# Kernel tuning notes

Measured on AMD Instinct MI355X. Metric: run time of the kernel, lower is better.

Reference implementation:

```python
import jax, jax.numpy as jnp
import numpy as np

N = 10000   # num nodes
E = 320000  # num edges (avg degree 32)
F = 128     # feat_size
H = 128     # hidden_size


def setup_inputs() -> dict:
    key = jax.random.key(0)
    ks = jax.random.split(key, 16)

    def p(k, shape, scale=0.05):
        return jax.random.normal(k, shape, jnp.float32) * scale

    inp = {
        "x": p(ks[0], (N, F), 1.0),
        "edge_index": jax.random.randint(ks[1], (2, E), 0, N),
    }
    # 6 SAGEConv layers: encoder (F->H, H->H), attr decoder (H->H, H->F),
    # struct decoder (H->H, H->N). Each has W_l (neighbor), b_l, W_r (root).
    dims = [(F, H), (H, H), (H, H), (H, F), (H, H), (H, N)]
    names = ["e1", "e2", "a1", "a2", "s1", "s2"]
    i = 2
    for name, (din, dout) in zip(names, dims):
        inp[f"Wl_{name}"] = p(ks[i], (din, dout))
        inp[f"bl_{name}"] = jnp.zeros((dout,), jnp.float32)
        inp[f"Wr_{name}"] = p(ks[i + 1], (din, dout))
        i += 2
    return inp


def sage(x, src, dst, Wl, bl, Wr, n):
    # PyG SAGEConv (aggr='mean'): mean of source-node features at each target,
    # then out = agg @ W_l + b + x @ W_r (root weight).
    msg = jax.ops.segment_sum(x[src], dst, num_segments=n)          # [n, din]
    deg = jax.ops.segment_sum(jnp.ones((src.shape[0],), x.dtype), dst, num_segments=n)
    agg = msg / jnp.maximum(deg, 1.0)[:, None]
    return agg @ Wl + bl + x @ Wr


def reference(x, edge_index,
              Wl_e1, bl_e1, Wr_e1, Wl_e2, bl_e2, Wr_e2,
              Wl_a1, bl_a1, Wr_a1, Wl_a2, bl_a2, Wr_a2,
              Wl_s1, bl_s1, Wr_s1, Wl_s2, bl_s2, Wr_s2):
    src, dst = edge_index[0], edge_index[1]
    n = x.shape[0]
    # Encoder (dropout is identity in eval mode)
    h = jax.nn.relu(sage(x, src, dst, Wl_e1, bl_e1, Wr_e1, n))
    h = jax.nn.relu(sage(h, src, dst, Wl_e2, bl_e2, Wr_e2, n))
    # Attribute decoder -> x_hat [N, F]
    xh = jax.nn.relu(sage(h, src, dst, Wl_a1, bl_a1, Wr_a1, n))
    xh = jax.nn.relu(sage(xh, src, dst, Wl_a2, bl_a2, Wr_a2, n))
    # Structure decoder -> [N, N], transposed as in the original
    s = jax.nn.relu(sage(h, src, dst, Wl_s1, bl_s1, Wr_s1, n))
    s = jax.nn.relu(sage(s, src, dst, Wl_s2, bl_s2, Wr_s2, n)).T
    return (s, xh)
```

## Files before the change

### kernel.cpp

```cpp
#include <hip/hip_runtime.h>
#include <hip/hip_bf16.h>

typedef unsigned short ushort_t;
typedef unsigned int uint_t;
typedef __attribute__((ext_vector_type(8))) short short8;
typedef __attribute__((ext_vector_type(4))) float float4v;

__device__ __forceinline__ float bf2f(ushort_t u) {
    union { uint_t i; float f; } c; c.i = ((uint_t)u) << 16; return c.f;
}
__device__ __forceinline__ ushort_t f2bf(float f) {
    union { float f; uint_t i; } c; c.f = f;
    uint_t x = c.i;
    uint_t r = x + 0x7fffu + ((x >> 16) & 1u);
    return (ushort_t)(r >> 16);
}

__device__ __forceinline__ void gl_lds16(const void* g, void* l) {
    __builtin_amdgcn_global_load_lds(
        (const __attribute__((address_space(1))) void*)g,
        (__attribute__((address_space(3))) void*)l, 16, 0, 0);
}

__device__ __forceinline__ void stv(float* p, float v) { *p = v; }
__device__ __forceinline__ void stv(ushort_t* p, float v) { *p = f2bf(v); }

__global__ __launch_bounds__(1024) void scan_kernel(
    const int* __restrict__ cnt, int* __restrict__ rowptr,
    int* __restrict__ cursor, float* __restrict__ deginv, int n) {
    __shared__ int sums[1024];
    const int t = threadIdx.x;
    const int per = (n + 1023) >> 10;
    const int b0 = t * per;
    int s = 0;
    for (int u = 0; u < per; u++) {
        int i = b0 + u;
        if (i < n) s += cnt[i];
    }
    sums[t] = s;
    __syncthreads();
    int x = s;
    for (int off = 1; off < 1024; off <<= 1) {
        int y = (t >= off) ? sums[t - off] : 0;
        __syncthreads();
        x += y;
        sums[t] = x;
        __syncthreads();
    }
    int run = x - s;
    for (int u = 0; u < per; u++) {
        int i = b0 + u;
        if (i < n) {
            int v = cnt[i];
            rowptr[i] = run;
            cursor[i] = run;
            deginv[i] = 1.0f / (float)(v > 0 ? v : 1);
            run += v;
        }
    }
    if (t == 1023) rowptr[n] = x;
}

__global__ void scatter_kernel(const int* __restrict__ srcv, const int* __restrict__ dstv,
                               int* __restrict__ cursor, int* __restrict__ srcs_sorted, int E) {
    int e = blockIdx.x * 256 + threadIdx.x;
    if (e < E) {
        int p = atomicAdd(&cursor[dstv[e]], 1);
        srcs_sorted[p] = srcv[e];
    }
}

struct W5 { const float* W0[5]; const float* W1[5]; };

__global__ __launch_bounds__(256) void setup_kernel(
    W5 wp, ushort_t* __restrict__ WT,
    const float* __restrict__ Ws2_0, const float* __restrict__ Ws2_1,
    ushort_t* __restrict__ WTs2, int Nout, int nbx,
    const int* __restrict__ dstv, int* __restrict__ cnt, int E) {
    __shared__ ushort_t tile[64][72];
    const int b = blockIdx.x;
    const int tid = threadIdx.x;
    if (b < 40) {
        const int bx = b & 1, by = (b >> 1) & 3, layer = b >> 3;
        const int i0 = bx * 64, k0 = by * 64;
        const float* W = (k0 < 128) ? (wp.W0[layer] + (size_t)k0 * 128)
                                    : (wp.W1[layer] + (size_t)(k0 - 128) * 128);
        ushort_t* WTb = WT + (size_t)layer * 128 * 256;
        const int li = tid & 63;
        const int kq = tid >> 6;
        const int gi = i0 + li;
        for (int k = kq; k < 64; k += 4)
            tile[li][k] = f2bf(W[(size_t)k * 128 + gi]);
        __syncthreads();
        for (int s = tid; s < 512; s += 256) {
            int r = s >> 3, ch = s & 7;
            *(short8*)(WTb + (size_t)(i0 + r) * 256 + k0 + ch * 8) = *(const short8*)&tile[r][ch * 8];
        }
    } else if (b < 40 + nbx * 4) {
        const int vt = b - 40;
        const int bx = vt % nbx, by = vt / nbx;
        const int i0 = bx * 64, k0 = by * 64;
        const float* W = (k0 < 128) ? (Ws2_0 + (size_t)k0 * Nout)
                                    : (Ws2_1 + (size_t)(k0 - 128) * Nout);
        const int li = tid & 63;
        const int kq = tid >> 6;
        const int gi = i0 + li;
        const bool ok = gi < Nout;
        for (int k = kq; k < 64; k += 4) {
            float v = ok ? W[(size_t)k * Nout + gi] : 0.f;
            tile[li][k] = f2bf(v);
        }
        __syncthreads();
        for (int s = tid; s < 512; s += 256) {
            int r = s >> 3, ch = s & 7;
            int gi2 = i0 + r;
            if (gi2 < Nout)
                *(short8*)(WTs2 + (size_t)gi2 * 256 + k0 + ch * 8) = *(const short8*)&tile[r][ch * 8];
        }
    } else {
        int e = (b - 40 - nbx * 4) * 256 + tid;
        if (e < E) atomicAdd(&cnt[dstv[e]], 1);
    }
}

template <typename TIN>
__device__ __forceinline__ float2 ld2(const TIN* act, size_t row, int t);
template <>
__device__ __forceinline__ float2 ld2<float>(const float* act, size_t row, int t) {
    return ((const float2*)act)[row * 64 + t];
}
template <>
__device__ __forceinline__ float2 ld2<ushort_t>(const ushort_t* act, size_t row, int t) {
    uint_t u = ((const uint_t*)act)[row * 64 + t];
    float2 r; r.x = bf2f((ushort_t)(u & 0xffffu)); r.y = bf2f((ushort_t)(u >> 16));
    return r;
}

template <typename TIN>
__global__ __launch_bounds__(256) void aggregate_kernel(
    const TIN* __restrict__ act, const int* __restrict__ srcs,
    const int* __restrict__ rowptr, const float* __restrict__ deginv,
    ushort_t* __restrict__ Acat, int N) {
    int node = blockIdx.x * 4 + (threadIdx.x >> 6);
    if (node >= N) return;
    int t = threadIdx.x & 63;
    int e0 = rowptr[node], e1 = rowptr[node + 1];
    float ax = 0.f, ay = 0.f;
    int e = e0;
    for (; e + 4 <= e1; e += 4) {
        int s0 = srcs[e], s1 = srcs[e + 1], s2 = srcs[e + 2], s3 = srcs[e + 3];
        float2 v0 = ld2(act, (size_t)s0, t);
        float2 v1 = ld2(act, (size_t)s1, t);
        float2 v2 = ld2(act, (size_t)s2, t);
        float2 v3 = ld2(act, (size_t)s3, t);
        ax += v0.x + v1.x + v2.x + v3.x;
        ay += v0.y + v1.y + v2.y + v3.y;
    }
    for (; e < e1; e++) {
        float2 v = ld2(act, (size_t)srcs[e], t);
        ax += v.x; ay += v.y;
    }
    float dinv = deginv[node];
    uint_t m = ((uint_t)f2bf(ay * dinv) << 16) | (uint_t)f2bf(ax * dinv);
    float2 self = ld2(act, (size_t)node, t);
    uint_t sf = ((uint_t)f2bf(self.y) << 16) | (uint_t)f2bf(self.x);
    ((uint_t*)Acat)[(size_t)node * 128 + t]      = m;
    ((uint_t*)Acat)[(size_t)node * 128 + 64 + t] = sf;
}

__global__ __launch_bounds__(256) void aggregate2_kernel(
    const ushort_t* __restrict__ act, const int* __restrict__ srcs,
    const int* __restrict__ rowptr, const float* __restrict__ deginv,
    ushort_t* __restrict__ AcatA, ushort_t* __restrict__ AcatS, int N) {
    int node = blockIdx.x * 4 + (threadIdx.x >> 6);
    if (node >= N) return;
    int t = threadIdx.x & 63;
    const uint_t* A = (const uint_t*)act;
    int e0 = rowptr[node], e1 = rowptr[node + 1];
    float ax = 0.f, ay = 0.f, sx = 0.f, sy = 0.f;
    int e = e0;
    for (; e + 4 <= e1; e += 4) {
        size_t r0 = (size_t)srcs[e] * 128,     r1 = (size_t)srcs[e + 1] * 128;
        size_t r2 = (size_t)srcs[e + 2] * 128, r3 = (size_t)srcs[e + 3] * 128;
        uint_t ua0 = A[r0 + t], us0 = A[r0 + 64 + t];
        uint_t ua1 = A[r1 + t], us1 = A[r1 + 64 + t];
        uint_t ua2 = A[r2 + t], us2 = A[r2 + 64 + t];
        uint_t ua3 = A[r3 + t], us3 = A[r3 + 64 + t];
        ax += bf2f((ushort_t)(ua0 & 0xffffu)) + bf2f((ushort_t)(ua1 & 0xffffu))
            + bf2f((ushort_t)(ua2 & 0xffffu)) + bf2f((ushort_t)(ua3 & 0xffffu));
        ay += bf2f((ushort_t)(ua0 >> 16))     + bf2f((ushort_t)(ua1 >> 16))
            + bf2f((ushort_t)(ua2 >> 16))     + bf2f((ushort_t)(ua3 >> 16));
        sx += bf2f((ushort_t)(us0 & 0xffffu)) + bf2f((ushort_t)(us1 & 0xffffu))
            + bf2f((ushort_t)(us2 & 0xffffu)) + bf2f((ushort_t)(us3 & 0xffffu));
        sy += bf2f((ushort_t)(us0 >> 16))     + bf2f((ushort_t)(us1 >> 16))
            + bf2f((ushort_t)(us2 >> 16))     + bf2f((ushort_t)(us3 >> 16));
    }
    for (; e < e1; e++) {
        size_t r0 = (size_t)srcs[e] * 128;
        uint_t ua0 = A[r0 + t], us0 = A[r0 + 64 + t];
        ax += bf2f((ushort_t)(ua0 & 0xffffu));
        ay += bf2f((ushort_t)(ua0 >> 16));
        sx += bf2f((ushort_t)(us0 & 0xffffu));
        sy += bf2f((ushort_t)(us0 >> 16));
    }
    float dinv = deginv[node];
    size_t rb = (size_t)node * 128;
    uint_t sa = A[rb + t], ss = A[rb + 64 + t];
    ((uint_t*)AcatA)[rb + t]      = ((uint_t)f2bf(ay * dinv) << 16) | (uint_t)f2bf(ax * dinv);
    ((uint_t*)AcatA)[rb + 64 + t] = sa;
    ((uint_t*)AcatS)[rb + t]      = ((uint_t)f2bf(sy * dinv) << 16) | (uint_t)f2bf(sx * dinv);
    ((uint_t*)AcatS)[rb + 64 + t] = ss;
}

template <bool BIAS_I, int TM, typename TOUT>
__device__ __forceinline__ void gemm_tile_body(
    char* smem, int pid_m, int pid_n,
    const ushort_t* __restrict__ A, const ushort_t* __restrict__ B,
    const float* __restrict__ bias, const float* __restrict__ bias2, int jsplit,
    TOUT* __restrict__ C, int rowsA, int rowsB) {
    constexpr int IMN = TM / 32;
    constexpr int NLD = IMN + 4;
    constexpr int ABYTES = TM * 128;
    constexpr int BBYTES = 128 * 128;

    const int i0 = pid_m * TM;
    const int j0 = pid_n * 128;

    const int tid  = threadIdx.x;
    const int lane = tid & 63;
    const int wid  = tid >> 6;
    const int wm = wid >> 1, wn = wid & 1;
    const int r16 = lane & 15, quad = lane >> 4;
    const int rsub = lane >> 3;
    const int csw  = (lane & 7) ^ rsub;

    float4v acc[IMN][4];
#pragma unroll
    for (int a = 0; a < IMN; a++)
#pragma unroll
        for (int b = 0; b < 4; b++) acc[a][b] = (float4v){0.f, 0.f, 0.f, 0.f};

    auto stage = [&](int buf, int kt) {
        ushort_t* Ad = (ushort_t*)(smem + buf * (ABYTES + BBYTES));
        ushort_t* Bd = (ushort_t*)(smem + buf * (ABYTES + BBYTES) + ABYTES);
        const int kbase = kt * 64 + csw * 8;
#pragma unroll
        for (int t = 0; t < IMN; t++) {
            const int w8 = (wid * IMN + t) * 8;
            int rA = min(i0 + w8 + rsub, rowsA - 1);
            gl_lds16(A + (size_t)rA * 256 + kbase, Ad + w8 * 64);
        }
#pragma unroll
        for (int t = 0; t < 4; t++) {
            const int w8 = (wid * 4 + t) * 8;
            int rB = min(j0 + w8 + rsub, rowsB - 1);
            gl_lds16(B + (size_t)rB * 256 + kbase, Bd + w8 * 64);
        }
    };

    stage(0, 0);
#pragma unroll
    for (int kt = 0; kt < 4; kt++) {
        if (kt < 3) {
            stage((kt + 1) & 1, kt + 1);
            asm volatile("s_waitcnt vmcnt(%0)" :: "n"(NLD) : "memory");
        } else {
            asm volatile("s_waitcnt vmcnt(0)" ::: "memory");
        }
        __builtin_amdgcn_s_barrier();
        asm volatile("" ::: "memory");
        const ushort_t* Ac = (const ushort_t*)(smem + (kt & 1) * (ABYTES + BBYTES));
        const ushort_t* Bc = Ac + ABYTES / 2;
#pragma unroll
        for (int ks = 0; ks < 2; ks++) {
            const int chb = ks * 4 + quad;
            const int sw = ((chb ^ (r16 & 7))) * 8;
            short8 af[IMN], bfr[4];
#pragma unroll
            for (int im = 0; im < IMN; im++)
                af[im] = *(const short8*)(Ac + (wm * (TM / 2) + im * 16 + r16) * 64 + sw);
#pragma unroll
            for (int jn = 0; jn < 4; jn++)
                bfr[jn] = *(const short8*)(Bc + (wn * 64 + jn * 16 + r16) * 64 + sw);
#pragma unroll
            for (int im = 0; im < IMN; im++)
#pragma unroll
                for (int jn = 0; jn < 4; jn++)
                    acc[im][jn] = __builtin_amdgcn_mfma_f32_16x16x32_bf16(
                        af[im], bfr[jn], acc[im][jn], 0, 0, 0);
        }
        if (kt < 3) {
            asm volatile("s_waitcnt lgkmcnt(0)" ::: "memory");
            __builtin_amdgcn_sched_barrier(0);
            __builtin_amdgcn_s_barrier();
            asm volatile("" ::: "memory");
        }
    }

    const int rows_lim = rowsA - i0;
    const int cols_lim = rowsB - j0;

    if constexpr (sizeof(TOUT) == 4) {
        float* T = (float*)smem;
        constexpr int NCH = TM / 32;
#pragma unroll
        for (int c = 0; c < NCH; c++) {
            const int crow = c * 32;
            __syncthreads();
            if (wm == crow / (TM / 2)) {
                const int imb = (crow - wm * (TM / 2)) / 16;
#pragma unroll
                for (int ii = 0; ii < 2; ii++) {
                    const int im = imb + ii;
#pragma unroll
                    for (int jn = 0; jn < 4; jn++) {
                        const int jl = wn * 64 + jn * 16 + r16;
                        float bj = 0.f;
                        if (!BIAS_I) {
                            int jg = j0 + jl;
                            bj = (jg >= jsplit) ? bias2[jg - jsplit] : bias[jg];
                        }
#pragma unroll
                        for (int r = 0; r < 4; r++) {
                            const int rl = ii * 16 + quad * 4 + r;
                            float bv = BIAS_I ? bias[min(i0 + crow + rl, rowsA - 1)] : bj;
                            T[rl * 132 + jl] = fmaxf(acc[im][jn][r] + bv, 0.f);
                        }
                    }
                }
            }
            __syncthreads();
            const int c4 = tid & 31, rl0 = tid >> 5;
#pragma unroll
            for (int s = 0; s < 4; s++) {
                const int rl = rl0 + s * 8;
                const int il = crow + rl;
                if (il < rows_lim) {
                    const int jl = c4 * 4;
                    float* dst = (float*)C + (size_t)(i0 + il) * rowsB + j0 + jl;
                    if (jl + 4 <= cols_lim) {
                        float4v vv = *(const float4v*)&T[rl * 132 + jl];
                        __builtin_nontemporal_store(vv, (float4v*)dst);
                    } else {
                        for (int jj = 0; jj < 4; jj++)
                            if (jl + jj < cols_lim) dst[jj] = T[rl * 132 + jl + jj];
                    }
                }
            }
        }
    } else {
#pragma unroll
        for (int im = 0; im < IMN; im++) {
#pragma unroll
            for (int jn = 0; jn < 4; jn++) {
                const int jl = wn * 64 + jn * 16 + r16;
                if (jl < cols_lim) {
                    float bj = 0.f;
                    if (!BIAS_I) {
                        int jg = j0 + jl;
                        bj = (jg >= jsplit) ? bias2[jg - jsplit] : bias[jg];
                    }
#pragma unroll
                    for (int r = 0; r < 4; r++) {
                        const int il = wm * (TM / 2) + im * 16 + quad * 4 + r;
                        if (il < rows_lim) {
                            float bv = BIAS_I ? bias[i0 + il] : bj;
                            float v = fmaxf(acc[im][jn][r] + bv, 0.f);
                            stv(C + (size_t)(i0 + il) * rowsB + (j0 + jl), v);
                        }
                    }
                }
            }
        }
    }
}

template <bool BIAS_I, int TM, typename TOUT>
__global__ __launch_bounds__(256) void gemm_nt_kernel(
    const ushort_t* __restrict__ A, const ushort_t* __restrict__ B,
    const float* __restrict__ bias, const float* __restrict__ bias2, int jsplit,
    TOUT* __restrict__ C, int rowsA, int rowsB, int tilesM, int tilesN) {
    __shared__ __align__(16) char smem[2 * (TM * 128 + 16384)];
    const int lin = blockIdx.x;
    const int GRP = 8;
    const int nig = GRP * tilesN;
    const int gidg = lin / nig;
    const int first_m = gidg * GRP;
    const int gsz = min(tilesM - first_m, GRP);
    const int in_grp = lin - gidg * nig;
    int pid_m = first_m + (in_grp % gsz);
    int pid_n = in_grp / gsz;
    gemm_tile_body<BIAS_I, TM, TOUT>(smem, pid_m, pid_n, A, B, bias, bias2, jsplit,
                                     C, rowsA, rowsB);
}

__global__ __launch_bounds__(256) void gemm_dual_kernel(
    const ushort_t* __restrict__ Aa, const ushort_t* __restrict__ Ba,
    const float* __restrict__ biasA, float* __restrict__ Ca, int rowsAa,
    const ushort_t* __restrict__ As, const ushort_t* __restrict__ Bs,
    const float* __restrict__ biasS, float* __restrict__ Cs, int rowsS,
    int tilesMs, int nA) {
    __shared__ __align__(16) char smem[65536];
    const int BIG = 1 << 30;
    if ((int)blockIdx.x < nA) {
        gemm_tile_body<false, 64, float>(smem, blockIdx.x, 0, Aa, Ba, biasA, nullptr, BIG,
                                         Ca, rowsAa, 128);
    } else {
        const int lin = blockIdx.x - nA;
        const int nwg = gridDim.x - nA;
        const int w = (lin & 7) * (nwg >> 3) + (lin >> 3);
        const int tM8 = (tilesMs + 7) >> 3;
        const int sg = w >> 6, is = w & 63;
        const int sgm = sg % tM8, sgn = sg / tM8;
        const int pid_m = sgm * 8 + (is & 7);
        const int pid_n = sgn * 8 + (is >> 3);
        if (pid_m >= tilesMs || pid_n >= tilesMs) return;
        gemm_tile_body<true, 128, float>(smem, pid_m, pid_n, As, Bs, biasS, nullptr, BIG,
                                         Cs, rowsS, rowsS);
    }
}

extern "C" void kernel_launch(void* const* d_in, const int* in_sizes, int n_in,
                              void* d_out, int out_size, void* d_ws, size_t ws_size,
                              hipStream_t stream) {
    const int N = in_sizes[18];
    const int E = in_sizes[1] / 2;

    const float* x = (const float*)d_in[0];
    const int* ei = (const int*)d_in[1];
    const int* srcv = ei;
    const int* dstv = ei + E;

    const float* Wl[6] = {(const float*)d_in[2],  (const float*)d_in[5],
                          (const float*)d_in[8],  (const float*)d_in[11],
                          (const float*)d_in[14], (const float*)d_in[17]};
    const float* bl[6] = {(const float*)d_in[3],  (const float*)d_in[6],
                          (const float*)d_in[9],  (const float*)d_in[12],
                          (const float*)d_in[15], (const float*)d_in[18]};
    const float* Wr[6] = {(const float*)d_in[4],  (const float*)d_in[7],
                          (const float*)d_in[10], (const float*)d_in[13],
                          (const float*)d_in[16], (const float*)d_in[19]};

    char* p = (char*)d_ws;
    auto carve = [&](size_t bytes) -> char* {
        char* q = p;
        p += (bytes + 255) & ~(size_t)255;
        return q;
    };
    int*      cnt    = (int*)carve((size_t)N * 4);
    int*      rowptr = (int*)carve((size_t)(N + 1) * 4);
    int*      cursor = (int*)carve((size_t)N * 4);
    float*    deginv = (float*)carve((size_t)N * 4);
    int*      srcs   = (int*)carve((size_t)E * 4);
    ushort_t* Acat   = (ushort_t*)carve((size_t)N * 256 * 2);
    ushort_t* AcatS  = (ushort_t*)carve((size_t)N * 256 * 2);
    ushort_t* hbA    = (ushort_t*)carve((size_t)N * 128 * 2);
    ushort_t* hbB    = (ushort_t*)carve((size_t)N * 128 * 2);
    ushort_t* hbC    = (ushort_t*)carve((size_t)N * 256 * 2);
    ushort_t* WTs2   = (ushort_t*)carve((size_t)N * 256 * 2);
    ushort_t* WsT    = (ushort_t*)carve((size_t)5 * 128 * 256 * 2);

    hipMemsetAsync(cnt, 0, (size_t)N * 4, stream);

    W5 w5;
    w5.W0[0] = Wl[0]; w5.W1[0] = Wr[0];
    w5.W0[1] = Wl[1]; w5.W1[1] = Wr[1];
    w5.W0[2] = Wl[2]; w5.W1[2] = Wr[2];
    w5.W0[3] = Wl[4]; w5.W1[3] = Wr[4];
    w5.W0[4] = Wl[3]; w5.W1[4] = Wr[3];
    const int nbx = (N + 63) / 64;
    const int histBlocks = (E + 255) / 256;
    setup_kernel<<<40 + nbx * 4 + histBlocks, 256, 0, stream>>>(
        w5, WsT, Wl[5], Wr[5], WTs2, N, nbx, dstv, cnt, E);
    scan_kernel<<<1, 1024, 0, stream>>>(cnt, rowptr, cursor, deginv, N);
    scatter_kernel<<<(E + 255) / 256, 256, 0, stream>>>(srcv, dstv, cursor, srcs, E);

    float* outp = (float*)d_out;
    float* xh_out = outp + (size_t)N * N;

    const int tM128 = (N + 127) / 128;
    const int tM64  = (N + 63) / 64;
    const int BIG = 1 << 30;

    aggregate_kernel<float><<<(N + 3) / 4, 256, 0, stream>>>(x, srcs, rowptr, deginv, Acat, N);
    gemm_nt_kernel<false, 64, ushort_t><<<tM64, 256, 0, stream>>>(
        Acat, WsT + 0 * 32768, bl[0], nullptr, BIG, hbA, N, 128, tM64, 1);
    aggregate_kernel<ushort_t><<<(N + 3) / 4, 256, 0, stream>>>(hbA, srcs, rowptr, deginv, Acat, N);
    gemm_nt_kernel<false, 64, ushort_t><<<tM64, 256, 0, stream>>>(
        Acat, WsT + 1 * 32768, bl[1], nullptr, BIG, hbB, N, 128, tM64, 1);
    aggregate_kernel<ushort_t><<<(N + 3) / 4, 256, 0, stream>>>(hbB, srcs, rowptr, deginv, Acat, N);
    gemm_nt_kernel<false, 64, ushort_t><<<tM64 * 2, 256, 0, stream>>>(
        Acat, WsT + 2 * 32768, bl[2], bl[4], 128, hbC, N, 256, tM64, 2);
    aggregate2_kernel<<<(N + 3) / 4, 256, 0, stream>>>(hbC, srcs, rowptr, deginv, Acat, AcatS, N);
    const int tM8 = (tM128 + 7) / 8;
    gemm_dual_kernel<<<tM64 + tM8 * tM8 * 64, 256, 0, stream>>>(
        Acat, WsT + 4 * 32768, bl[3], xh_out, N,
        WTs2, AcatS, bl[5], outp, N, tM128, tM64);

    (void)n_in; (void)out_size; (void)ws_size;
}
```

Measured before the change: 640.7 us.

## Fuse neighbor mean aggregation into SAGE GEMM tiles via LDS-staged A operand

Replaces the separate aggregate and GEMM kernels for the first three layers and the attribute-decoder output layer with a fused kernel. Each block gathers and averages neighbor rows for its 64-node tile directly into a swizzled LDS A buffer, then runs the MFMA GEMM against streamed weights. This removes the Acat round-trip through global memory and several launches. The cost is that the gather now runs per column tile, so the 256-wide layer aggregates twice. Occupancy is also lower because each block holds 64KB of LDS and does latency-bound gathers inside the GEMM block.

```diff
diff --git a/kernel.cpp b/kernel.cpp
--- a/kernel.cpp
+++ b/kernel.cpp
@@ -24,6 +24,22 @@
 
 __device__ __forceinline__ void stv(float* p, float v) { *p = v; }
 __device__ __forceinline__ void stv(ushort_t* p, float v) { *p = f2bf(v); }
+
+__device__ __forceinline__ float2 ld2g(const float* act, size_t row, int su, int ou, int t) {
+    return ((const float2*)act)[row * su + ou + t];
+}
+__device__ __forceinline__ float2 ld2g(const ushort_t* act, size_t row, int su, int ou, int t) {
+    uint_t u = ((const uint_t*)act)[row * su + ou + t];
+    float2 r; r.x = bf2f((ushort_t)(u & 0xffffu)); r.y = bf2f((ushort_t)(u >> 16));
+    return r;
+}
+__device__ __forceinline__ uint_t self_pack(const float* act, size_t row, int su, int ou, int t) {
+    float2 s = ((const float2*)act)[row * su + ou + t];
+    return ((uint_t)f2bf(s.y) << 16) | (uint_t)f2bf(s.x);
+}
+__device__ __forceinline__ uint_t self_pack(const ushort_t* act, size_t row, int su, int ou, int t) {
+    return ((const uint_t*)act)[row * su + ou + t];
+}
 
 __global__ __launch_bounds__(1024) void scan_kernel(
     const int* __restrict__ cnt, int* __restrict__ rowptr,
@@ -123,73 +139,22 @@
     }
 }
 
-template <typename TIN>
-__device__ __forceinline__ float2 ld2(const TIN* act, size_t row, int t);
-template <>
-__device__ __forceinline__ float2 ld2<float>(const float* act, size_t row, int t) {
-    return ((const float2*)act)[row * 64 + t];
-}
-template <>
-__device__ __forceinline__ float2 ld2<ushort_t>(const ushort_t* act, size_t row, int t) {
-    uint_t u = ((const uint_t*)act)[row * 64 + t];
-    float2 r; r.x = bf2f((ushort_t)(u & 0xffffu)); r.y = bf2f((ushort_t)(u >> 16));
-    return r;
-}
-
-template <typename TIN>
-__global__ __launch_bounds__(256) void aggregate_kernel(
-    const TIN* __restrict__ act, const int* __restrict__ srcs,
-    const int* __restrict__ rowptr, const float* __restrict__ deginv,
-    ushort_t* __restrict__ Acat, int N) {
-    int node = blockIdx.x * 4 + (threadIdx.x >> 6);
-    if (node >= N) return;
-    int t = threadIdx.x & 63;
-    int e0 = rowptr[node], e1 = rowptr[node + 1];
-    float ax = 0.f, ay = 0.f;
-    int e = e0;
-    for (; e + 4 <= e1; e += 4) {
-        int s0 = srcs[e], s1 = srcs[e + 1], s2 = srcs[e + 2], s3 = srcs[e + 3];
-        float2 v0 = ld2(act, (size_t)s0, t);
-        float2 v1 = ld2(act, (size_t)s1, t);
-        float2 v2 = ld2(act, (size_t)s2, t);
-        float2 v3 = ld2(act, (size_t)s3, t);
-        ax += v0.x + v1.x + v2.x + v3.x;
-        ay += v0.y + v1.y + v2.y + v3.y;
-    }
-    for (; e < e1; e++) {
-        float2 v = ld2(act, (size_t)srcs[e], t);
-        ax += v.x; ay += v.y;
-    }
-    float dinv = deginv[node];
-    uint_t m = ((uint_t)f2bf(ay * dinv) << 16) | (uint_t)f2bf(ax * dinv);
-    float2 self = ld2(act, (size_t)node, t);
-    uint_t sf = ((uint_t)f2bf(self.y) << 16) | (uint_t)f2bf(self.x);
-    ((uint_t*)Acat)[(size_t)node * 128 + t]      = m;
-    ((uint_t*)Acat)[(size_t)node * 128 + 64 + t] = sf;
-}
-
-__global__ __launch_bounds__(256) void aggregate2_kernel(
+__global__ __launch_bounds__(256) void aggS_kernel(
     const ushort_t* __restrict__ act, const int* __restrict__ srcs,
     const int* __restrict__ rowptr, const float* __restrict__ deginv,
-    ushort_t* __restrict__ AcatA, ushort_t* __restrict__ AcatS, int N) {
+    ushort_t* __restrict__ AcatS, int N) {
     int node = blockIdx.x * 4 + (threadIdx.x >> 6);
     if (node >= N) return;
     int t = threadIdx.x & 63;
     const uint_t* A = (const uint_t*)act;
     int e0 = rowptr[node], e1 = rowptr[node + 1];
-    float ax = 0.f, ay = 0.f, sx = 0.f, sy = 0.f;
+    float sx = 0.f, sy = 0.f;
     int e = e0;
     for (; e + 4 <= e1; e += 4) {
         size_t r0 = (size_t)srcs[e] * 128,     r1 = (size_t)srcs[e + 1] * 128;
         size_t r2 = (size_t)srcs[e + 2] * 128, r3 = (size_t)srcs[e + 3] * 128;
-        uint_t ua0 = A[r0 + t], us0 = A[r0 + 64 + t];
-        uint_t ua1 = A[r1 + t], us1 = A[r1 + 64 + t];
-        uint_t ua2 = A[r2 + t], us2 = A[r2 + 64 + t];
-        uint_t ua3 = A[r3 + t], us3 = A[r3 + 64 + t];
-        ax += bf2f((ushort_t)(ua0 & 0xffffu)) + bf2f((ushort_t)(ua1 & 0xffffu))
-            + bf2f((ushort_t)(ua2 & 0xffffu)) + bf2f((ushort_t)(ua3 & 0xffffu));
-        ay += bf2f((ushort_t)(ua0 >> 16))     + bf2f((ushort_t)(ua1 >> 16))
-            + bf2f((ushort_t)(ua2 >> 16))     + bf2f((ushort_t)(ua3 >> 16));
+        uint_t us0 = A[r0 + 64 + t], us1 = A[r1 + 64 + t];
+        uint_t us2 = A[r2 + 64 + t], us3 = A[r3 + 64 + t];
         sx += bf2f((ushort_t)(us0 & 0xffffu)) + bf2f((ushort_t)(us1 & 0xffffu))
             + bf2f((ushort_t)(us2 & 0xffffu)) + bf2f((ushort_t)(us3 & 0xffffu));
         sy += bf2f((ushort_t)(us0 >> 16))     + bf2f((ushort_t)(us1 >> 16))
@@ -197,17 +162,13 @@
     }
     for (; e < e1; e++) {
         size_t r0 = (size_t)srcs[e] * 128;
-        uint_t ua0 = A[r0 + t], us0 = A[r0 + 64 + t];
-        ax += bf2f((ushort_t)(ua0 & 0xffffu));
-        ay += bf2f((ushort_t)(ua0 >> 16));
+        uint_t us0 = A[r0 + 64 + t];
         sx += bf2f((ushort_t)(us0 & 0xffffu));
         sy += bf2f((ushort_t)(us0 >> 16));
     }
     float dinv = deginv[node];
     size_t rb = (size_t)node * 128;
-    uint_t sa = A[rb + t], ss = A[rb + 64 + t];
-    ((uint_t*)AcatA)[rb + t]      = ((uint_t)f2bf(ay * dinv) << 16) | (uint_t)f2bf(ax * dinv);
-    ((uint_t*)AcatA)[rb + 64 + t] = sa;
+    uint_t ss = A[rb + 64 + t];
     ((uint_t*)AcatS)[rb + t]      = ((uint_t)f2bf(sy * dinv) << 16) | (uint_t)f2bf(sx * dinv);
     ((uint_t*)AcatS)[rb + 64 + t] = ss;
 }
@@ -375,36 +336,212 @@
     }
 }
 
-template <bool BIAS_I, int TM, typename TOUT>
-__global__ __launch_bounds__(256) void gemm_nt_kernel(
-    const ushort_t* __restrict__ A, const ushort_t* __restrict__ B,
-    const float* __restrict__ bias, const float* __restrict__ bias2, int jsplit,
-    TOUT* __restrict__ C, int rowsA, int rowsB, int tilesM, int tilesN) {
-    __shared__ __align__(16) char smem[2 * (TM * 128 + 16384)];
-    const int lin = blockIdx.x;
-    const int GRP = 8;
-    const int nig = GRP * tilesN;
-    const int gidg = lin / nig;
-    const int first_m = gidg * GRP;
-    const int gsz = min(tilesM - first_m, GRP);
-    const int in_grp = lin - gidg * nig;
-    int pid_m = first_m + (in_grp % gsz);
-    int pid_n = in_grp / gsz;
-    gemm_tile_body<BIAS_I, TM, TOUT>(smem, pid_m, pid_n, A, B, bias, bias2, jsplit,
-                                     C, rowsA, rowsB);
+template <typename TIN, typename TOUT>
+__device__ __forceinline__ void fused_tile_body(
+    char* smem, int pid_m, int pid_n,
+    const TIN* __restrict__ act, int su, int ou,
+    const int* __restrict__ srcs, const int* __restrict__ rowptr,
+    const float* __restrict__ deginv,
+    const ushort_t* __restrict__ Bw, const float* __restrict__ bias,
+    const float* __restrict__ bias2, int jsplit,
+    TOUT* __restrict__ C, int rowsA, int rowsB) {
+
+    ushort_t* Afull = (ushort_t*)smem;
+    ushort_t* Blds  = (ushort_t*)(smem + 32768);
+
+    const int i0 = pid_m * 64;
+    const int j0 = pid_n * 128;
+    const int tid  = threadIdx.x;
+    const int lane = tid & 63;
+    const int wid  = tid >> 6;
+    const int wm = wid >> 1, wn = wid & 1;
+    const int r16 = lane & 15, quad = lane >> 4;
+    const int rsub = lane >> 3;
+    const int csw  = (lane & 7) ^ rsub;
+    const int t = lane;
+
+    const int slot_base = (t & 31) >> 2;
+    for (int k = 0; k < 16; k++) {
+        const int r = wid * 16 + k;
+        const int gnode = min(i0 + r, rowsA - 1);
+        int e0 = rowptr[gnode], e1 = rowptr[gnode + 1];
+        float ax = 0.f, ay = 0.f;
+        int e = e0;
+        for (; e + 4 <= e1; e += 4) {
+            int s0 = srcs[e], s1 = srcs[e + 1], s2 = srcs[e + 2], s3 = srcs[e + 3];
+            float2 v0 = ld2g(act, (size_t)s0, su, ou, t);
+            float2 v1 = ld2g(act, (size_t)s1, su, ou, t);
+            float2 v2 = ld2g(act, (size_t)s2, su, ou, t);
+            float2 v3 = ld2g(act, (size_t)s3, su, ou, t);
+            ax += v0.x + v1.x + v2.x + v3.x;
+            ay += v0.y + v1.y + v2.y + v3.y;
+        }
+        for (; e < e1; e++) {
+            float2 v = ld2g(act, (size_t)srcs[e], su, ou, t);
+            ax += v.x; ay += v.y;
+        }
+        float dinv = deginv[gnode];
+        uint_t m  = ((uint_t)f2bf(ay * dinv) << 16) | (uint_t)f2bf(ax * dinv);
+        uint_t sf = self_pack(act, (size_t)gnode, su, ou, t);
+        const int slot = slot_base ^ (r & 7);
+        const int idx = r * 128 + ((t >> 5) << 5) + (slot << 2) + (t & 3);
+        ((uint_t*)Afull)[idx]      = m;
+        ((uint_t*)Afull)[idx + 64] = sf;
+    }
+    __syncthreads();
+
+    float4v acc[2][4];
+#pragma unroll
+    for (int a = 0; a < 2; a++)
+#pragma unroll
+        for (int b = 0; b < 4; b++) acc[a][b] = (float4v){0.f, 0.f, 0.f, 0.f};
+
+    auto stageB = [&](int buf, int kt) {
+        ushort_t* Bd = Blds + buf * 8192;
+        const int kbase = kt * 64 + csw * 8;
+#pragma unroll
+        for (int w = 0; w < 4; w++) {
+            const int w8 = (wid * 4 + w) * 8;
+            int rB = min(j0 + w8 + rsub, rowsB - 1);
+            gl_lds16(Bw + (size_t)rB * 256 + kbase, Bd + w8 * 64);
+        }
+    };
+
+    stageB(0, 0);
+#pragma unroll
+    for (int kt = 0; kt < 4; kt++) {
+        if (kt < 3) {
+            stageB((kt + 1) & 1, kt + 1);
+            asm volatile("s_waitcnt vmcnt(%0)" :: "n"(4) : "memory");
+        } else {
+            asm volatile("s_waitcnt vmcnt(0)" ::: "memory");
+        }
+        __builtin_amdgcn_s_barrier();
+        asm volatile("" ::: "memory");
+        const ushort_t* Bc = Blds + (kt & 1) * 8192;
+#pragma unroll
+        for (int ks = 0; ks < 2; ks++) {
+            const int chb = ks * 4 + quad;
+            const int sw = ((chb ^ (r16 & 7))) * 8;
+            short8 af[2], bfr[4];
+#pragma unroll
+            for (int im = 0; im < 2; im++)
+                af[im] = *(const short8*)(Afull + (wm * 32 + im * 16 + r16) * 256 + kt * 64 + sw);
+#pragma unroll
+            for (int jn = 0; jn < 4; jn++)
+                bfr[jn] = *(const short8*)(Bc + (wn * 64 + jn * 16 + r16) * 64 + sw);
+#pragma unroll
+            for (int im = 0; im < 2; im++)
+#pragma unroll
+                for (int jn = 0; jn < 4; jn++)
+                    acc[im][jn] = __builtin_amdgcn_mfma_f32_16x16x32_bf16(
+                        af[im], bfr[jn], acc[im][jn], 0, 0, 0);
+        }
+        if (kt < 3) {
+            asm volatile("s_waitcnt lgkmcnt(0)" ::: "memory");
+            __builtin_amdgcn_sched_barrier(0);
+            __builtin_amdgcn_s_barrier();
+            asm volatile("" ::: "memory");
+        }
+    }
+
+    const int rows_lim = rowsA - i0;
+    const int cols_lim = rowsB - j0;
+
+    if constexpr (sizeof(TOUT) == 4) {
+        float* T = (float*)smem;
+#pragma unroll
+        for (int c = 0; c < 2; c++) {
+            const int crow = c * 32;
+            __syncthreads();
+            if (wm == c) {
+#pragma unroll
+                for (int ii = 0; ii < 2; ii++) {
+                    const int im = ii;
+#pragma unroll
+                    for (int jn = 0; jn < 4; jn++) {
+                        const int jl = wn * 64 + jn * 16 + r16;
+                        int jg = j0 + jl;
+                        float bj = (jg >= jsplit) ? bias2[jg - jsplit] : bias[jg];
+#pragma unroll
+                        for (int r = 0; r < 4; r++) {
+                            const int rl = ii * 16 + quad * 4 + r;
+                            T[rl * 132 + jl] = fmaxf(acc[im][jn][r] + bj, 0.f);
+                        }
+                    }
+                }
+            }
+            __syncthreads();
+            const int c4 = tid & 31, rl0 = tid >> 5;
+#pragma unroll
+            for (int s = 0; s < 4; s++) {
+                const int rl = rl0 + s * 8;
+                const int il = crow + rl;
+                if (il < rows_lim) {
+                    const int jl = c4 * 4;
+                    float* dst = (float*)C + (size_t)(i0 + il) * rowsB + j0 + jl;
+                    if (jl + 4 <= cols_lim) {
+                        float4v vv = *(const float4v*)&T[rl * 132 + jl];
+                        __builtin_nontemporal_store(vv, (float4v*)dst);
+                    } else {
+                        for (int jj = 0; jj < 4; jj++)
+                            if (jl + jj < cols_lim) dst[jj] = T[rl * 132 + jl + jj];
+                    }
+                }
+            }
+        }
+    } else {
+#pragma unroll
+        for (int im = 0; im < 2; im++) {
+#pragma unroll
+            for (int jn = 0; jn < 4; jn++) {
+                const int jl = wn * 64 + jn * 16 + r16;
+                if (jl < cols_lim) {
+                    int jg = j0 + jl;
+                    float bj = (jg >= jsplit) ? bias2[jg - jsplit] : bias[jg];
+#pragma unroll
+                    for (int r = 0; r < 4; r++) {
+                        const int il = wm * 32 + im * 16 + quad * 4 + r;
+                        if (il < rows_lim) {
+                            float v = fmaxf(acc[im][jn][r] + bj, 0.f);
+                            stv(C + (size_t)(i0 + il) * rowsB + (j0 + jl), v);
+                        }
+                    }
+                }
+            }
+        }
+    }
+}
+
+template <typename TIN>
+__global__ __launch_bounds__(256) void fused_agg_gemm_kernel(
+    const TIN* __restrict__ act, int su, int ou,
+    const int* __restrict__ srcs, const int* __restrict__ rowptr,
+    const float* __restrict__ deginv,
+    const ushort_t* __restrict__ Bw, const float* __restrict__ bias,
+    const float* __restrict__ bias2, int jsplit,
+    ushort_t* __restrict__ C, int rowsA, int rowsB, int tilesN) {
+    __shared__ __align__(16) char smem[65536];
+    const int pid_m = blockIdx.x / tilesN;
+    const int pid_n = blockIdx.x % tilesN;
+    fused_tile_body<TIN, ushort_t>(smem, pid_m, pid_n, act, su, ou, srcs, rowptr,
+                                   deginv, Bw, bias, bias2, jsplit, C, rowsA, rowsB);
 }
 
 __global__ __launch_bounds__(256) void gemm_dual_kernel(
-    const ushort_t* __restrict__ Aa, const ushort_t* __restrict__ Ba,
-    const float* __restrict__ biasA, float* __restrict__ Ca, int rowsAa,
+    const ushort_t* __restrict__ actA, const int* __restrict__ srcs,
+    const int* __restrict__ rowptr, const float* __restrict__ deginv,
+    const ushort_t* __restrict__ Ba, const float* __restrict__ biasA,
+    float* __restrict__ Ca, int nA,
     const ushort_t* __restrict__ As, const ushort_t* __restrict__ Bs,
-    const float* __restrict__ biasS, float* __restrict__ Cs, int rowsS,
-    int tilesMs, int nA) {
+    const float* __restrict__ biasS, float* __restrict__ Cs,
+    int N, int tilesMs) {
     __shared__ __align__(16) char smem[65536];
     const int BIG = 1 << 30;
     if ((int)blockIdx.x < nA) {
-        gemm_tile_body<false, 64, float>(smem, blockIdx.x, 0, Aa, Ba, biasA, nullptr, BIG,
-                                         Ca, rowsAa, 128);
+        fused_tile_body<ushort_t, float>(smem, blockIdx.x, 0, actA, 128, 0,
+                                         srcs, rowptr, deginv, Ba, biasA, nullptr, BIG,
+                                         Ca, N, 128);
     } else {
         const int lin = blockIdx.x - nA;
         const int nwg = gridDim.x - nA;
@@ -416,7 +553,7 @@
         const int pid_n = sgn * 8 + (is >> 3);
         if (pid_m >= tilesMs || pid_n >= tilesMs) return;
         gemm_tile_body<true, 128, float>(smem, pid_m, pid_n, As, Bs, biasS, nullptr, BIG,
-                                         Cs, rowsS, rowsS);
+                                         Cs, N, N);
     }
 }
 
@@ -452,7 +589,6 @@
     int*      cursor = (int*)carve((size_t)N * 4);
     float*    deginv = (float*)carve((size_t)N * 4);
     int*      srcs   = (int*)carve((size_t)E * 4);
-    ushort_t* Acat   = (ushort_t*)carve((size_t)N * 256 * 2);
     ushort_t* AcatS  = (ushort_t*)carve((size_t)N * 256 * 2);
     ushort_t* hbA    = (ushort_t*)carve((size_t)N * 128 * 2);
     ushort_t* hbB    = (ushort_t*)carve((size_t)N * 128 * 2);
@@ -482,20 +618,20 @@
     const int tM64  = (N + 63) / 64;
     const int BIG = 1 << 30;
 
-    aggregate_kernel<float><<<(N + 3) / 4, 256, 0, stream>>>(x, srcs, rowptr, deginv, Acat, N);
-    gemm_nt_kernel<false, 64, ushort_t><<<tM64, 256, 0, stream>>>(
-        Acat, WsT + 0 * 32768, bl[0], nullptr, BIG, hbA, N, 128, tM64, 1);
-    aggregate_kernel<ushort_t><<<(N + 3) / 4, 256, 0, stream>>>(hbA, srcs, rowptr, deginv, Acat, N);
-    gemm_nt_kernel<false, 64, ushort_t><<<tM64, 256, 0, stream>>>(
-        Acat, WsT + 1 * 32768, bl[1], nullptr, BIG, hbB, N, 128, tM64, 1);
-    aggregate_kernel<ushort_t><<<(N + 3) / 4, 256, 0, stream>>>(hbB, srcs, rowptr, deginv, Acat, N);
-    gemm_nt_kernel<false, 64, ushort_t><<<tM64 * 2, 256, 0, stream>>>(
-        Acat, WsT + 2 * 32768, bl[2], bl[4], 128, hbC, N, 256, tM64, 2);
-    aggregate2_kernel<<<(N + 3) / 4, 256, 0, stream>>>(hbC, srcs, rowptr, deginv, Acat, AcatS, N);
+    fused_agg_gemm_kernel<float><<<tM64, 256, 0, stream>>>(
+        x, 64, 0, srcs, rowptr, deginv, WsT + 0 * 32768, bl[0], nullptr, BIG,
+        hbA, N, 128, 1);
+    fused_agg_gemm_kernel<ushort_t><<<tM64, 256, 0, stream>>>(
+        hbA, 64, 0, srcs, rowptr, deginv, WsT + 1 * 32768, bl[1], nullptr, BIG,
+        hbB, N, 128, 1);
+    fused_agg_gemm_kernel<ushort_t><<<tM64 * 2, 256, 0, stream>>>(
+        hbB, 64, 0, srcs, rowptr, deginv, WsT + 2 * 32768, bl[2], bl[4], 128,
+        hbC, N, 256, 2);
+    aggS_kernel<<<(N + 3) / 4, 256, 0, stream>>>(hbC, srcs, rowptr, deginv, AcatS, N);
     const int tM8 = (tM128 + 7) / 8;
     gemm_dual_kernel<<<tM64 + tM8 * tM8 * 64, 256, 0, stream>>>(
-        Acat, WsT + 4 * 32768, bl[3], xh_out, N,
-        WTs2, AcatS, bl[5], outp, N, tM128, tM64);
+        hbC, srcs, rowptr, deginv, WsT + 4 * 32768, bl[3], xh_out, tM64,
+        WTs2, AcatS, bl[5], outp, N, tM128);
 
     (void)n_in; (void)out_size; (void)ws_size;
 }
```

Result: slower. 827.5 us (+29.2%).
